# Kernel optimization log

Hardware: AMD Instinct MI355X
Metric: run time of the kernel (lower is better)

Reference implementation:

```python
import jax, jax.numpy as jnp
import numpy as np

BATCH, E = 4096, 8
DIMS = [512, 1024, 1024, 512]


def setup_inputs() -> dict:
    key = jax.random.key(0)
    ks = jax.random.split(key, 8)
    inp = {
        'weight_blend': jax.random.uniform(ks[0], (BATCH, E), dtype=jnp.float32),
        'x': jax.random.normal(ks[1], (BATCH, DIMS[0]), dtype=jnp.float32),
    }
    for i in range(3):
        inp[f'W{i}'] = jax.random.normal(ks[2 + i], (E, DIMS[i + 1], DIMS[i]), dtype=jnp.float32)
        inp[f'B{i}'] = jnp.zeros((E, DIMS[i + 1]), dtype=jnp.float32)
    return inp


def _blended_layer(weight_blend, x, W, B):
    # Fused form of: weight = sum_e blend[b,e]*W[e]; y = bmm(weight, x) + sum_e blend[b,e]*B[e]
    # Computed as sum_e blend_e * (W_e @ x) without materializing (batch,out,in).
    y = jnp.einsum('eoi,bi->beo', W, x)          # per-expert GEMM, (B,E,out)
    y = jnp.einsum('be,beo->bo', weight_blend, y)  # blend combine
    return y + weight_blend @ B                   # blended bias (B,out)


def reference(weight_blend, x, W0, B0, W1, B1, W2, B2):
    # Dropout with keep_prob=0.0 is identity in eval mode; activations: elu, elu, linear.
    h = jax.nn.elu(_blended_layer(weight_blend, x, W0, B0))
    h = jax.nn.elu(_blended_layer(weight_blend, h, W1, B1))
    out = _blended_layer(weight_blend, h, W2, B2)
    return out
```

## Files before the change

### kernel.cpp

```cpp
#include <hip/hip_runtime.h>
#include <cstdint>
#include <cstddef>

typedef __bf16 bf16x8 __attribute__((ext_vector_type(8)));
typedef float f32x4 __attribute__((ext_vector_type(4)));
typedef unsigned short u16;
typedef unsigned short u16x8 __attribute__((ext_vector_type(8)));

#define BATCH 4096
#define NE 8

__device__ __forceinline__ u16 f2bf(float f) {
  union { float f; uint32_t u; } v; v.f = f;
  uint32_t u = v.u;
  u += 0x7fffu + ((u >> 16) & 1u);
  return (u16)(u >> 16);
}

__device__ __forceinline__ float bf2f(u16 u) {
  union { uint32_t u; float f; } v; v.u = ((uint32_t)u) << 16;
  return v.f;
}

__device__ __forceinline__ void cast8(const float* src, u16* dst) {
  const float4* p = (const float4*)src;
  float4 a = p[0], b = p[1];
  u16x8 o;
  o[0] = f2bf(a.x); o[1] = f2bf(a.y); o[2] = f2bf(a.z); o[3] = f2bf(a.w);
  o[4] = f2bf(b.x); o[5] = f2bf(b.y); o[6] = f2bf(b.z); o[7] = f2bf(b.w);
  *(u16x8*)dst = o;
}

__device__ __forceinline__ void conv_w_chunk(const float* __restrict__ W,
                                             u16* __restrict__ Bt,
                                             int N, int K0, int chunk) {
  int per_row = K0 >> 3;
  int rid = chunk / per_row;
  int i0 = (chunk - rid * per_row) << 3;
  int e = rid / N;
  int o = rid - e * N;
  cast8(W + (size_t)rid * K0 + i0,
        Bt + (size_t)o * ((size_t)NE * K0) + (size_t)e * K0 + i0);
}

__global__ void prep_kernel(const float* __restrict__ x,
                            const float* __restrict__ W0,
                            const float* __restrict__ W1,
                            const float* __restrict__ W2,
                            u16* __restrict__ h0, u16* __restrict__ Bt0,
                            u16* __restrict__ Bt1, u16* __restrict__ Bt2) {
  int t = blockIdx.x * blockDim.x + threadIdx.x;
  const int C0 = BATCH * 512 / 8;
  const int C1 = C0 + NE * 1024 * 512 / 8;
  const int C2 = C1 + NE * 1024 * 1024 / 8;
  if (t < C0) {
    cast8(x + (size_t)t * 8, h0 + (size_t)t * 8);
  } else if (t < C1) {
    conv_w_chunk(W0, Bt0, 1024, 512, t - C0);
  } else if (t < C2) {
    conv_w_chunk(W1, Bt1, 1024, 1024, t - C1);
  } else {
    conv_w_chunk(W2, Bt2, 512, 1024, t - C2);
  }
}

template<int SLICES, bool ELU_ACT, bool OUT_BF16>
__global__ void combineS_kernel(const u16* __restrict__ P,
                                const float* __restrict__ blend,
                                const float* __restrict__ Bias,
                                void* __restrict__ outp, int N) {
  int t = blockIdx.x * blockDim.x + threadIdx.x;
  int per_row = N >> 3;
  int b = t / per_row;
  int i0 = (t - b * per_row) << 3;
  const size_t slice = (size_t)BATCH * N;
  float v[8] = {0, 0, 0, 0, 0, 0, 0, 0};
  #pragma unroll
  for (int s = 0; s < SLICES; ++s) {
    u16x8 pv = *(const u16x8*)(P + (size_t)s * slice + (size_t)b * N + i0);
    #pragma unroll
    for (int j = 0; j < 8; ++j) v[j] += bf2f(pv[j]);
  }
  const float4* blp = (const float4*)(blend + b * NE);
  float4 u0 = blp[0], u1 = blp[1];
  float bl[8] = {u0.x, u0.y, u0.z, u0.w, u1.x, u1.y, u1.z, u1.w};
  #pragma unroll
  for (int e = 0; e < NE; ++e) {
    const float4* bp = (const float4*)(Bias + (size_t)e * N + i0);
    float4 ba = bp[0], bb = bp[1];
    float bv[8] = {ba.x, ba.y, ba.z, ba.w, bb.x, bb.y, bb.z, bb.w};
    #pragma unroll
    for (int j = 0; j < 8; ++j) v[j] += bl[e] * bv[j];
  }
  if (ELU_ACT) {
    #pragma unroll
    for (int j = 0; j < 8; ++j) v[j] = v[j] > 0.f ? v[j] : expm1f(v[j]);
  }
  if (OUT_BF16) {
    u16x8 o;
    #pragma unroll
    for (int j = 0; j < 8; ++j) o[j] = f2bf(v[j]);
    *(u16x8*)((u16*)outp + (size_t)b * N + i0) = o;
  } else {
    float4* op = (float4*)((float*)outp + (size_t)b * N + i0);
    op[0] = (float4){v[0], v[1], v[2], v[3]};
    op[1] = (float4){v[4], v[5], v[6], v[7]};
  }
}

#define GL2LDS(g, l) __builtin_amdgcn_global_load_lds( \
    (__attribute__((address_space(1))) void*)(g),      \
    (__attribute__((address_space(3))) void*)(l), 16, 0, 0)

template<int K0, int EPB>
__global__ __launch_bounds__(256, 2)
void gemm_fold_kernel(const u16* __restrict__ h, const u16* __restrict__ Bt,
                      const float* __restrict__ blend,
                      u16* __restrict__ P, int N) {
  __shared__ __align__(16) u16 Hs[128 * 64];
  __shared__ __align__(16) u16 Bs[128 * 64];
  __shared__ float bls[128 * 9];

  const int tid  = threadIdx.x;
  const int w    = tid >> 6, lane = tid & 63;
  const int wm   = w >> 1,   wn   = w & 1;
  const int lrow = lane & 15, quad = lane >> 4;

  const int row0 = blockIdx.x * 128;
  const int col0 = blockIdx.y * 128;
  const int e0   = blockIdx.z * EPB;
  const int EK   = K0 * NE;

  {
    const float4 bv = ((const float4*)(blend + (size_t)row0 * NE))[tid];
    int row = tid >> 1, c0 = (tid & 1) * 4;
    bls[row * 9 + c0 + 0] = bv.x;
    bls[row * 9 + c0 + 1] = bv.y;
    bls[row * 9 + c0 + 2] = bv.z;
    bls[row * 9 + c0 + 3] = bv.w;
  }

  const int trow = tid >> 3;
  const int tcol = (tid & 7) ^ (trow & 7);
  const u16* gH = h + (size_t)(row0 + trow) * K0 + (tcol << 3);
  const u16* gB = Bt + (size_t)(col0 + trow) * EK + (size_t)e0 * K0 + (tcol << 3);
  u16* lH = &Hs[tid * 8];
  u16* lB = &Bs[tid * 8];

  const int xr = lrow & 7;
  const u16* fH[2][4];
  const u16* fB[2][4];
  #pragma unroll
  for (int kc = 0; kc < 2; ++kc)
    #pragma unroll
    for (int i = 0; i < 4; ++i) {
      fH[kc][i] = &Hs[(wm * 64 + i * 16 + lrow) * 64 + (((kc * 4 + quad) ^ xr) << 3)];
      fB[kc][i] = &Bs[(wn * 64 + i * 16 + lrow) * 64 + (((kc * 4 + quad) ^ xr) << 3)];
    }

  f32x4 acc[4][4];
  #pragma unroll
  for (int i = 0; i < 4; ++i)
    #pragma unroll
    for (int j = 0; j < 4; ++j) acc[i][j] = (f32x4){0.f, 0.f, 0.f, 0.f};

  #pragma unroll 1
  for (int ee = 0; ee < EPB; ++ee) {
    f32x4 acc2[4][4];
    #pragma unroll
    for (int i = 0; i < 4; ++i)
      #pragma unroll
      for (int j = 0; j < 4; ++j) acc2[i][j] = (f32x4){0.f, 0.f, 0.f, 0.f};

    const u16* pH = gH;
    const u16* pB = gB + (size_t)ee * K0;

    for (int it = 0; it < K0 / 64; ++it) {
      #pragma unroll
      for (int i = 0; i < 4; ++i) {
        GL2LDS(pH + (size_t)(32 * i) * K0, lH + 2048 * i);
        GL2LDS(pB + (size_t)(32 * i) * EK, lB + 2048 * i);
      }
      pH += 64; pB += 64;
      __syncthreads();

      #pragma unroll
      for (int kc = 0; kc < 2; ++kc) {
        bf16x8 hf[4], bfr[4];
        #pragma unroll
        for (int i = 0; i < 4; ++i) hf[i] = *(const bf16x8*)fH[kc][i];
        #pragma unroll
        for (int j = 0; j < 4; ++j) bfr[j] = *(const bf16x8*)fB[kc][j];
        #pragma unroll
        for (int i = 0; i < 4; ++i)
          #pragma unroll
          for (int j = 0; j < 4; ++j)
            acc2[i][j] = __builtin_amdgcn_mfma_f32_16x16x32_bf16(hf[i], bfr[j], acc2[i][j], 0, 0, 0);
      }
      __syncthreads();
    }

    #pragma unroll
    for (int mt = 0; mt < 4; ++mt) {
      float bl[4];
      #pragma unroll
      for (int r = 0; r < 4; ++r)
        bl[r] = bls[(wm * 64 + mt * 16 + quad * 4 + r) * 9 + (e0 + ee)];
      #pragma unroll
      for (int nt = 0; nt < 4; ++nt)
        #pragma unroll
        for (int r = 0; r < 4; ++r)
          acc[mt][nt][r] += bl[r] * acc2[mt][nt][r];
    }
  }

  u16* Ps = P + (size_t)blockIdx.z * ((size_t)BATCH * N);
  u16* ls = &Hs[w * 2048];
  #pragma unroll
  for (int half = 0; half < 2; ++half) {
    #pragma unroll
    for (int mh = 0; mh < 2; ++mh) {
      int mt = half * 2 + mh;
      #pragma unroll
      for (int r = 0; r < 4; ++r) {
        int rloc = mh * 16 + quad * 4 + r;
        #pragma unroll
        for (int nt = 0; nt < 4; ++nt) {
          int col = nt * 16 + lrow;
          int c8 = (col >> 3) ^ (rloc & 7);
          ls[rloc * 64 + (c8 << 3) + (col & 7)] = f2bf(acc[mt][nt][r]);
        }
      }
    }
    #pragma unroll
    for (int p = 0; p < 4; ++p) {
      int rloc = p * 8 + (lane >> 3);
      int c8 = (lane & 7) ^ (rloc & 7);
      u16x8 v = *(const u16x8*)&ls[rloc * 64 + (c8 << 3)];
      int row = row0 + wm * 64 + half * 32 + rloc;
      int colg = col0 + wn * 64 + ((lane & 7) << 3);
      *(u16x8*)&Ps[(size_t)row * N + colg] = v;
    }
  }
}

extern "C" void kernel_launch(void* const* d_in, const int* in_sizes, int n_in,
                              void* d_out, int out_size, void* d_ws, size_t ws_size,
                              hipStream_t stream) {
  const float* blend = (const float*)d_in[0];
  const float* x  = (const float*)d_in[1];
  const float* W0 = (const float*)d_in[2];
  const float* B0 = (const float*)d_in[3];
  const float* W1 = (const float*)d_in[4];
  const float* B1 = (const float*)d_in[5];
  const float* W2 = (const float*)d_in[6];
  const float* B2 = (const float*)d_in[7];
  float* out = (float*)d_out;

  char* ws = (char*)d_ws;
  u16* hA  = (u16*)ws;
  u16* h1  = (u16*)(ws + 8388608);
  u16* Bt0 = (u16*)(ws + 16777216);
  u16* Bt1 = (u16*)(ws + 25165824);
  u16* Bt2 = (u16*)(ws + 41943040);
  u16* P   = (u16*)(ws + 50331648);

  prep_kernel<<<9216, 256, 0, stream>>>(x, W0, W1, W2, hA, Bt0, Bt1, Bt2);

  gemm_fold_kernel<512, 4><<<dim3(32, 8, 2), 256, 0, stream>>>(hA, Bt0, blend, P, 1024);
  combineS_kernel<2, true, true><<<2048, 256, 0, stream>>>(P, blend, B0, h1, 1024);

  gemm_fold_kernel<1024, 4><<<dim3(32, 8, 2), 256, 0, stream>>>(h1, Bt1, blend, P, 1024);
  combineS_kernel<2, true, true><<<2048, 256, 0, stream>>>(P, blend, B1, hA, 1024);

  gemm_fold_kernel<1024, 2><<<dim3(32, 4, 4), 256, 0, stream>>>(hA, Bt2, blend, P, 512);
  combineS_kernel<4, false, false><<<1024, 256, 0, stream>>>(P, blend, B2, out, 512);
}
```

Measured before the change: 285.3 us.

## Pipeline blended GEMM with triple-buffered LDS and blend-scaled A tiles

Replaces the per-expert GEMM with an inner accumulator and epilogue blend by a single flattened K loop over experts. The blend weight is applied to the activation tile as it is written to LDS, so one accumulator suffices. The kernel uses 512 threads with a 256x128 tile, triple-buffered LDS, and register-staged A loads with explicit vmcnt waits, barriers and setprio, so global loads overlap MFMA work. In exchange, A values are rounded to bf16 after scaling, LDS use per block goes up, and occupancy may drop.

```diff
diff --git a/kernel.cpp b/kernel.cpp
--- a/kernel.cpp
+++ b/kernel.cpp
@@ -112,51 +112,79 @@
     (__attribute__((address_space(1))) void*)(g),      \
     (__attribute__((address_space(3))) void*)(l), 16, 0, 0)
 
+#define SBAR  asm volatile("s_barrier" ::: "memory")
+#define LGKM0 asm volatile("s_waitcnt lgkmcnt(0)" ::: "memory")
+#define VMW3  asm volatile("s_waitcnt vmcnt(3)" ::: "memory")
+#define VMW0  asm volatile("s_waitcnt vmcnt(0)" ::: "memory")
+
+__device__ __forceinline__ uint4 scale8(uint4 d, float s) {
+  uint32_t* pi = (uint32_t*)&d;
+  uint4 o;
+  uint32_t* po = (uint32_t*)&o;
+  #pragma unroll
+  for (int i = 0; i < 4; ++i) {
+    uint32_t wv = pi[i];
+    float lo = __uint_as_float(wv << 16) * s;
+    float hi = __uint_as_float(wv & 0xffff0000u) * s;
+    uint32_t pk;
+    asm("v_cvt_pk_bf16_f32 %0, %1, %2" : "=v"(pk) : "v"(lo), "v"(hi));
+    po[i] = pk;
+  }
+  return o;
+}
+
 template<int K0, int EPB>
-__global__ __launch_bounds__(256, 2)
-void gemm_fold_kernel(const u16* __restrict__ h, const u16* __restrict__ Bt,
+__global__ __launch_bounds__(512, 2)
+void gemm_pipe_kernel(const u16* __restrict__ h, const u16* __restrict__ Bt,
                       const float* __restrict__ blend,
                       u16* __restrict__ P, int N) {
-  __shared__ __align__(16) u16 Hs[128 * 64];
-  __shared__ __align__(16) u16 Bs[128 * 64];
-  __shared__ float bls[128 * 9];
+  constexpr int TPE  = K0 / 32;
+  constexpr int LTPE = (K0 == 512) ? 4 : 5;
+  constexpr int NT   = EPB * TPE;
+  const int EK = NE * K0;
+
+  __shared__ __align__(16) char SM[73728];
+  __shared__ float bls[256 * 9];
 
   const int tid  = threadIdx.x;
-  const int w    = tid >> 6, lane = tid & 63;
-  const int wm   = w >> 1,   wn   = w & 1;
+  const int lane = tid & 63, w = tid >> 6;
+  const int wm   = w >> 1, wn = w & 1;
   const int lrow = lane & 15, quad = lane >> 4;
 
-  const int row0 = blockIdx.x * 128;
+  const int row0 = blockIdx.x * 256;
   const int col0 = blockIdx.y * 128;
   const int e0   = blockIdx.z * EPB;
-  const int EK   = K0 * NE;
 
   {
     const float4 bv = ((const float4*)(blend + (size_t)row0 * NE))[tid];
-    int row = tid >> 1, c0 = (tid & 1) * 4;
-    bls[row * 9 + c0 + 0] = bv.x;
-    bls[row * 9 + c0 + 1] = bv.y;
-    bls[row * 9 + c0 + 2] = bv.z;
-    bls[row * 9 + c0 + 3] = bv.w;
-  }
-
-  const int trow = tid >> 3;
-  const int tcol = (tid & 7) ^ (trow & 7);
-  const u16* gH = h + (size_t)(row0 + trow) * K0 + (tcol << 3);
-  const u16* gB = Bt + (size_t)(col0 + trow) * EK + (size_t)e0 * K0 + (tcol << 3);
-  u16* lH = &Hs[tid * 8];
-  u16* lB = &Bs[tid * 8];
-
-  const int xr = lrow & 7;
-  const u16* fH[2][4];
-  const u16* fB[2][4];
-  #pragma unroll
-  for (int kc = 0; kc < 2; ++kc)
-    #pragma unroll
-    for (int i = 0; i < 4; ++i) {
-      fH[kc][i] = &Hs[(wm * 64 + i * 16 + lrow) * 64 + (((kc * 4 + quad) ^ xr) << 3)];
-      fB[kc][i] = &Bs[(wn * 64 + i * 16 + lrow) * 64 + (((kc * 4 + quad) ^ xr) << 3)];
-    }
+    int r = tid >> 1, c = (tid & 1) * 4;
+    bls[r * 9 + c + 0] = bv.x;
+    bls[r * 9 + c + 1] = bv.y;
+    bls[r * 9 + c + 2] = bv.z;
+    bls[r * 9 + c + 3] = bv.w;
+  }
+
+  const int sr  = tid >> 2, sc = tid & 3;
+  const int csw = sc ^ (sr & 3);
+  const uint32_t wA0 = (uint32_t)(sr * 64 + (csw << 4));
+  const uint32_t wA1 = (uint32_t)((128 + sr) * 64 + (csw << 4));
+  const int blo0 = sr * 9, blo1 = (128 + sr) * 9;
+
+  const u16* gA0 = h + (size_t)(row0 + sr) * K0 + sc * 8;
+  const u16* gA1 = gA0 + (size_t)128 * K0;
+  const u16* gB  = Bt + (size_t)(col0 + sr) * EK + csw * 8;
+
+#define KCOL(T) (((T) & (TPE - 1)) * 32)
+#define KOFF(T) ((e0 + ((T) >> LTPE)) * K0 + KCOL(T))
+
+  const int xq = quad ^ (lrow & 3);
+  uint32_t aoff[4], boff[4];
+  #pragma unroll
+  for (int i = 0; i < 4; ++i)
+    aoff[i] = (uint32_t)((wm * 64 + i * 16 + lrow) * 64 + (xq << 4));
+  #pragma unroll
+  for (int j = 0; j < 4; ++j)
+    boff[j] = (uint32_t)((wn * 64 + j * 16 + lrow) * 64 + (xq << 4));
 
   f32x4 acc[4][4];
   #pragma unroll
@@ -164,58 +192,81 @@
     #pragma unroll
     for (int j = 0; j < 4; ++j) acc[i][j] = (f32x4){0.f, 0.f, 0.f, 0.f};
 
+  __syncthreads();
+
+  uint32_t c0 = 0, c1 = 16384, c2 = 32768;
+  uint4 sE0, sE1, sO0, sO1;
+
+  GL2LDS(gB + KOFF(0), SM + 49152 + (c0 >> 1) + (size_t)tid * 16);
+  sE0 = *(const uint4*)(gA0 + KCOL(0));
+  sE1 = *(const uint4*)(gA1 + KCOL(0));
+  GL2LDS(gB + KOFF(1), SM + 49152 + (c1 >> 1) + (size_t)tid * 16);
+  sO0 = *(const uint4*)(gA0 + KCOL(1));
+  sO1 = *(const uint4*)(gA1 + KCOL(1));
+  {
+    const float bl0 = bls[blo0 + e0], bl1 = bls[blo1 + e0];
+    *(uint4*)(SM + c0 + wA0) = scale8(sE0, bl0);
+    *(uint4*)(SM + c0 + wA1) = scale8(sE1, bl1);
+  }
+  VMW0; LGKM0; SBAR;
+
+#define TILE(T, CUR, NXT, NN, LD0, LD1, WR0, WR1)                               \
+  {                                                                             \
+    bf16x8 bfr[4], afr[2];                                                      \
+    _Pragma("unroll")                                                           \
+    for (int j = 0; j < 4; ++j)                                                 \
+      bfr[j] = *(const bf16x8*)(SM + 49152 + ((CUR) >> 1) + boff[j]);           \
+    _Pragma("unroll")                                                           \
+    for (int i = 0; i < 2; ++i)                                                 \
+      afr[i] = *(const bf16x8*)(SM + (CUR) + aoff[i]);                          \
+    if ((T) + 2 < NT) {                                                         \
+      GL2LDS(gB + KOFF((T) + 2), SM + 49152 + ((NN) >> 1) + (size_t)tid * 16);  \
+      LD0 = *(const uint4*)(gA0 + KCOL((T) + 2));                               \
+      LD1 = *(const uint4*)(gA1 + KCOL((T) + 2));                               \
+    }                                                                           \
+    __builtin_amdgcn_s_setprio(1);                                              \
+    _Pragma("unroll")                                                           \
+    for (int i = 0; i < 2; ++i)                                                 \
+      _Pragma("unroll")                                                         \
+      for (int j = 0; j < 4; ++j)                                               \
+        acc[i][j] = __builtin_amdgcn_mfma_f32_16x16x32_bf16(afr[i], bfr[j],     \
+                                                            acc[i][j], 0, 0, 0);\
+    __builtin_amdgcn_s_setprio(0);                                              \
+    if ((T) + 1 < NT) {                                                         \
+      const int e_ = e0 + (((T) + 1) >> LTPE);                                  \
+      const float bl0_ = bls[blo0 + e_], bl1_ = bls[blo1 + e_];                 \
+      *(uint4*)(SM + (NXT) + wA0) = scale8(WR0, bl0_);                          \
+      *(uint4*)(SM + (NXT) + wA1) = scale8(WR1, bl1_);                          \
+    }                                                                           \
+    SBAR;                                                                       \
+    _Pragma("unroll")                                                           \
+    for (int i = 0; i < 2; ++i)                                                 \
+      afr[i] = *(const bf16x8*)(SM + (CUR) + aoff[2 + i]);                      \
+    __builtin_amdgcn_s_setprio(1);                                              \
+    _Pragma("unroll")                                                           \
+    for (int i = 0; i < 2; ++i)                                                 \
+      _Pragma("unroll")                                                         \
+      for (int j = 0; j < 4; ++j)                                               \
+        acc[2 + i][j] = __builtin_amdgcn_mfma_f32_16x16x32_bf16(                \
+            afr[i], bfr[j], acc[2 + i][j], 0, 0, 0);                            \
+    __builtin_amdgcn_s_setprio(0);                                              \
+    if ((T) + 2 < NT) { VMW3; } else { VMW0; }                                  \
+    LGKM0;                                                                      \
+    SBAR;                                                                       \
+  }
+
   #pragma unroll 1
-  for (int ee = 0; ee < EPB; ++ee) {
-    f32x4 acc2[4][4];
-    #pragma unroll
-    for (int i = 0; i < 4; ++i)
-      #pragma unroll
-      for (int j = 0; j < 4; ++j) acc2[i][j] = (f32x4){0.f, 0.f, 0.f, 0.f};
-
-    const u16* pH = gH;
-    const u16* pB = gB + (size_t)ee * K0;
-
-    for (int it = 0; it < K0 / 64; ++it) {
-      #pragma unroll
-      for (int i = 0; i < 4; ++i) {
-        GL2LDS(pH + (size_t)(32 * i) * K0, lH + 2048 * i);
-        GL2LDS(pB + (size_t)(32 * i) * EK, lB + 2048 * i);
-      }
-      pH += 64; pB += 64;
-      __syncthreads();
-
-      #pragma unroll
-      for (int kc = 0; kc < 2; ++kc) {
-        bf16x8 hf[4], bfr[4];
-        #pragma unroll
-        for (int i = 0; i < 4; ++i) hf[i] = *(const bf16x8*)fH[kc][i];
-        #pragma unroll
-        for (int j = 0; j < 4; ++j) bfr[j] = *(const bf16x8*)fB[kc][j];
-        #pragma unroll
-        for (int i = 0; i < 4; ++i)
-          #pragma unroll
-          for (int j = 0; j < 4; ++j)
-            acc2[i][j] = __builtin_amdgcn_mfma_f32_16x16x32_bf16(hf[i], bfr[j], acc2[i][j], 0, 0, 0);
-      }
-      __syncthreads();
-    }
-
-    #pragma unroll
-    for (int mt = 0; mt < 4; ++mt) {
-      float bl[4];
-      #pragma unroll
-      for (int r = 0; r < 4; ++r)
-        bl[r] = bls[(wm * 64 + mt * 16 + quad * 4 + r) * 9 + (e0 + ee)];
-      #pragma unroll
-      for (int nt = 0; nt < 4; ++nt)
-        #pragma unroll
-        for (int r = 0; r < 4; ++r)
-          acc[mt][nt][r] += bl[r] * acc2[mt][nt][r];
-    }
-  }
+  for (int t = 0; t < NT; t += 2) {
+    TILE(t,     c0, c1, c2, sE0, sE1, sO0, sO1);
+    TILE(t + 1, c1, c2, c0, sO0, sO1, sE0, sE1);
+    const uint32_t tmp = c2; c2 = c1; c1 = c0; c0 = tmp;
+  }
+#undef TILE
+#undef KOFF
+#undef KCOL
 
   u16* Ps = P + (size_t)blockIdx.z * ((size_t)BATCH * N);
-  u16* ls = &Hs[w * 2048];
+  u16* ls = (u16*)SM + w * 2048;
   #pragma unroll
   for (int half = 0; half < 2; ++half) {
     #pragma unroll
@@ -267,12 +318,12 @@
 
   prep_kernel<<<9216, 256, 0, stream>>>(x, W0, W1, W2, hA, Bt0, Bt1, Bt2);
 
-  gemm_fold_kernel<512, 4><<<dim3(32, 8, 2), 256, 0, stream>>>(hA, Bt0, blend, P, 1024);
+  gemm_pipe_kernel<512, 4><<<dim3(16, 8, 2), 512, 0, stream>>>(hA, Bt0, blend, P, 1024);
   combineS_kernel<2, true, true><<<2048, 256, 0, stream>>>(P, blend, B0, h1, 1024);
 
-  gemm_fold_kernel<1024, 4><<<dim3(32, 8, 2), 256, 0, stream>>>(h1, Bt1, blend, P, 1024);
+  gemm_pipe_kernel<1024, 4><<<dim3(16, 8, 2), 512, 0, stream>>>(h1, Bt1, blend, P, 1024);
   combineS_kernel<2, true, true><<<2048, 256, 0, stream>>>(P, blend, B1, hA, 1024);
 
-  gemm_fold_kernel<1024, 2><<<dim3(32, 4, 4), 256, 0, stream>>>(hA, Bt2, blend, P, 512);
+  gemm_pipe_kernel<1024, 2><<<dim3(16, 4, 4), 512, 0, stream>>>(hA, Bt2, blend, P, 512);
   combineS_kernel<4, false, false><<<1024, 256, 0, stream>>>(P, blend, B2, out, 512);
 }
```

Measured after the change: 376.7 us. 1.32x slower.

## Fold blend weights into expanded activations and use pipelined 256x256 split-K GEMM

Applied to the files above, without the earlier changes.

Pre-scales activations by each expert's blend weight (writing an expanded B x 8K bf16 activation), so each layer becomes a single plain GEMM over K=8*K0 against the expert-concatenated weights, with no per-expert epilogue. Replaces the old 128x128 GEMM with a 512-thread 256x256 tile kernel that double-buffers LDS with direct global-to-LDS loads, interleaved staging, explicit vmcnt waits and setprio, split across K slices. This removes the per-expert blend epilogue and improves data reuse and load/compute overlap. In exchange it multiplies activation memory traffic by 8 and needs more split-K partial slices in the combine step.

```diff
diff --git a/kernel.cpp b/kernel.cpp
--- a/kernel.cpp
+++ b/kernel.cpp
@@ -43,18 +43,33 @@
         Bt + (size_t)o * ((size_t)NE * K0) + (size_t)e * K0 + i0);
 }
 
-__global__ void prep_kernel(const float* __restrict__ x,
+__global__ void prep_kernel(const float* __restrict__ blend,
+                            const float* __restrict__ x,
                             const float* __restrict__ W0,
                             const float* __restrict__ W1,
                             const float* __restrict__ W2,
-                            u16* __restrict__ h0, u16* __restrict__ Bt0,
+                            u16* __restrict__ hh0, u16* __restrict__ Bt0,
                             u16* __restrict__ Bt1, u16* __restrict__ Bt2) {
   int t = blockIdx.x * blockDim.x + threadIdx.x;
   const int C0 = BATCH * 512 / 8;
   const int C1 = C0 + NE * 1024 * 512 / 8;
   const int C2 = C1 + NE * 1024 * 1024 / 8;
   if (t < C0) {
-    cast8(x + (size_t)t * 8, h0 + (size_t)t * 8);
+    int b = t >> 6, i0 = (t & 63) << 3;
+    const float4* xp = (const float4*)(x + (size_t)b * 512 + i0);
+    float4 a = xp[0], c = xp[1];
+    float xv[8] = {a.x, a.y, a.z, a.w, c.x, c.y, c.z, c.w};
+    const float4* blp = (const float4*)(blend + (size_t)b * NE);
+    float4 u0 = blp[0], u1 = blp[1];
+    float bl[8] = {u0.x, u0.y, u0.z, u0.w, u1.x, u1.y, u1.z, u1.w};
+    u16* dst = hh0 + (size_t)b * 4096 + i0;
+    #pragma unroll
+    for (int e = 0; e < NE; ++e) {
+      u16x8 o;
+      #pragma unroll
+      for (int j = 0; j < 8; ++j) o[j] = f2bf(bl[e] * xv[j]);
+      *(u16x8*)(dst + (size_t)e * 512) = o;
+    }
   } else if (t < C1) {
     conv_w_chunk(W0, Bt0, 1024, 512, t - C0);
   } else if (t < C2) {
@@ -64,7 +79,7 @@
   }
 }
 
-template<int SLICES, bool ELU_ACT, bool OUT_BF16>
+template<int SLICES, bool ELU_ACT, int OM>
 __global__ void combineS_kernel(const u16* __restrict__ P,
                                 const float* __restrict__ blend,
                                 const float* __restrict__ Bias,
@@ -96,11 +111,16 @@
     #pragma unroll
     for (int j = 0; j < 8; ++j) v[j] = v[j] > 0.f ? v[j] : expm1f(v[j]);
   }
-  if (OUT_BF16) {
-    u16x8 o;
-    #pragma unroll
-    for (int j = 0; j < 8; ++j) o[j] = f2bf(v[j]);
-    *(u16x8*)((u16*)outp + (size_t)b * N + i0) = o;
+  if (OM == 1) {
+    u16* hh = (u16*)outp;
+    size_t base = (size_t)b * ((size_t)NE * N) + i0;
+    #pragma unroll
+    for (int e = 0; e < NE; ++e) {
+      u16x8 o;
+      #pragma unroll
+      for (int j = 0; j < 8; ++j) o[j] = f2bf(bl[e] * v[j]);
+      *(u16x8*)(hh + base + (size_t)e * N) = o;
+    }
   } else {
     float4* op = (float4*)((float*)outp + (size_t)b * N + i0);
     op[0] = (float4){v[0], v[1], v[2], v[3]};
@@ -112,115 +132,121 @@
     (__attribute__((address_space(1))) void*)(g),      \
     (__attribute__((address_space(3))) void*)(l), 16, 0, 0)
 
-template<int K0, int EPB>
-__global__ __launch_bounds__(256, 2)
-void gemm_fold_kernel(const u16* __restrict__ h, const u16* __restrict__ Bt,
-                      const float* __restrict__ blend,
-                      u16* __restrict__ P, int N) {
-  __shared__ __align__(16) u16 Hs[128 * 64];
-  __shared__ __align__(16) u16 Bs[128 * 64];
-  __shared__ float bls[128 * 9];
+#define SBAR  asm volatile("s_barrier" ::: "memory")
+#define VMW6  asm volatile("s_waitcnt vmcnt(6)" ::: "memory")
+
+template<int NT>
+__global__ __launch_bounds__(512, 2)
+void gemm8p_kernel(const u16* __restrict__ A, const u16* __restrict__ B,
+                   u16* __restrict__ P, int N, int KTOT, int KSL) {
+  __shared__ __align__(16) char SM[131072];
 
   const int tid  = threadIdx.x;
-  const int w    = tid >> 6, lane = tid & 63;
-  const int wm   = w >> 1,   wn   = w & 1;
+  const int lane = tid & 63, w = tid >> 6;
+  const int wm   = w >> 2, wn = w & 3;
   const int lrow = lane & 15, quad = lane >> 4;
 
-  const int row0 = blockIdx.x * 128;
-  const int col0 = blockIdx.y * 128;
-  const int e0   = blockIdx.z * EPB;
-  const int EK   = K0 * NE;
-
-  {
-    const float4 bv = ((const float4*)(blend + (size_t)row0 * NE))[tid];
-    int row = tid >> 1, c0 = (tid & 1) * 4;
-    bls[row * 9 + c0 + 0] = bv.x;
-    bls[row * 9 + c0 + 1] = bv.y;
-    bls[row * 9 + c0 + 2] = bv.z;
-    bls[row * 9 + c0 + 3] = bv.w;
-  }
-
-  const int trow = tid >> 3;
-  const int tcol = (tid & 7) ^ (trow & 7);
-  const u16* gH = h + (size_t)(row0 + trow) * K0 + (tcol << 3);
-  const u16* gB = Bt + (size_t)(col0 + trow) * EK + (size_t)e0 * K0 + (tcol << 3);
-  u16* lH = &Hs[tid * 8];
-  u16* lB = &Bs[tid * 8];
+  const int row0 = blockIdx.x * 256;
+  const int col0 = blockIdx.y * 256;
+  const size_t kb0 = (size_t)blockIdx.z * KSL;
+
+  const int sr = tid >> 3, sc = tid & 7;
+  const int tcol = sc ^ (sr & 7);
+  const u16* gA = A + ((size_t)(row0 + sr) * KTOT + kb0 + (tcol << 3));
+  const u16* gB = B + ((size_t)(col0 + sr) * KTOT + kb0 + (tcol << 3));
+
+#define STA(T, q, BUF) GL2LDS(gA + (size_t)(64 * (q)) * KTOT + (size_t)(T) * 64, \
+                              SM + (BUF) * 65536 + (q) * 8192 + (size_t)tid * 16)
+#define STB(T, q, BUF) GL2LDS(gB + (size_t)(64 * (q)) * KTOT + (size_t)(T) * 64, \
+                              SM + (BUF) * 65536 + 32768 + (q) * 8192 + (size_t)tid * 16)
 
   const int xr = lrow & 7;
-  const u16* fH[2][4];
-  const u16* fB[2][4];
+  const uint32_t arow = (uint32_t)((wm * 128 + lrow) * 128);
+  const uint32_t brow = (uint32_t)((wn * 64 + lrow) * 128);
+  uint32_t ch[2];
+  ch[0] = (uint32_t)((quad ^ xr) << 4);
+  ch[1] = (uint32_t)(((4 + quad) ^ xr) << 4);
+
+  f32x4 acc[8][4];
   #pragma unroll
-  for (int kc = 0; kc < 2; ++kc)
-    #pragma unroll
-    for (int i = 0; i < 4; ++i) {
-      fH[kc][i] = &Hs[(wm * 64 + i * 16 + lrow) * 64 + (((kc * 4 + quad) ^ xr) << 3)];
-      fB[kc][i] = &Bs[(wn * 64 + i * 16 + lrow) * 64 + (((kc * 4 + quad) ^ xr) << 3)];
-    }
-
-  f32x4 acc[4][4];
+  for (int i = 0; i < 8; ++i)
+    #pragma unroll
+    for (int j = 0; j < 4; ++j) acc[i][j] = (f32x4){0.f, 0.f, 0.f, 0.f};
+
+  STA(0, 0, 0); STA(0, 1, 0); STA(0, 2, 0); STA(0, 3, 0);
+  STB(0, 0, 0); STB(0, 1, 0); STB(0, 2, 0); STB(0, 3, 0);
+  STB(1, 0, 1); STB(1, 1, 1); STB(1, 2, 1); STB(1, 3, 1);
+  STA(1, 0, 1); STA(1, 2, 1);
+  VMW6;
+  SBAR;
+
+#define PHASE(q, CUR, RDB, STAGES)                                              \
+  {                                                                             \
+    if (RDB) {                                                                  \
+      _Pragma("unroll")                                                         \
+      for (int nt = 0; nt < 4; ++nt)                                            \
+        _Pragma("unroll")                                                       \
+        for (int kc = 0; kc < 2; ++kc)                                          \
+          bfr[nt][kc] = *(const bf16x8*)(SM + (CUR) + 32768 + brow +            \
+                                         nt * 2048 + ch[kc]);                   \
+    }                                                                           \
+    bf16x8 af[2][2];                                                            \
+    _Pragma("unroll")                                                           \
+    for (int m2 = 0; m2 < 2; ++m2)                                              \
+      _Pragma("unroll")                                                         \
+      for (int kc = 0; kc < 2; ++kc)                                            \
+        af[m2][kc] = *(const bf16x8*)(SM + (CUR) + arow +                       \
+                                      ((q) * 2 + m2) * 2048 + ch[kc]);          \
+    STAGES;                                                                     \
+    SBAR;                                                                       \
+    __builtin_amdgcn_s_setprio(1);                                              \
+    _Pragma("unroll")                                                           \
+    for (int kc = 0; kc < 2; ++kc)                                              \
+      _Pragma("unroll")                                                         \
+      for (int m2 = 0; m2 < 2; ++m2)                                            \
+        _Pragma("unroll")                                                       \
+        for (int nt = 0; nt < 4; ++nt)                                          \
+          acc[(q) * 2 + m2][nt] = __builtin_amdgcn_mfma_f32_16x16x32_bf16(      \
+              af[m2][kc], bfr[nt][kc], acc[(q) * 2 + m2][nt], 0, 0, 0);         \
+    __builtin_amdgcn_s_setprio(0);                                              \
+  }
+
+  constexpr int NIT = NT / 2;
+  #pragma unroll 1
+  for (int j = 0; j < NIT; ++j) {
+    const int u = 2 * j;
+    const bool sg = (u + 2 < NT);
+    bf16x8 bfr[4][2];
+    PHASE(0, 0, true,  { STA(u + 1, 1, 1); STA(u + 1, 3, 1); });
+    SBAR;
+    PHASE(1, 0, false, { if (sg) { STB(u + 2, 0, 0); STB(u + 2, 1, 0); } });
+    SBAR;
+    PHASE(2, 0, false, { if (sg) { STA(u + 2, 0, 0); STA(u + 2, 2, 0); } });
+    SBAR;
+    PHASE(3, 0, false, { if (sg) { STB(u + 2, 2, 0); STB(u + 2, 3, 0); } });
+    VMW6;
+    SBAR;
+    PHASE(0, 65536, true,  { if (sg) { STA(u + 2, 1, 0); STA(u + 2, 3, 0); } });
+    SBAR;
+    PHASE(1, 65536, false, { if (sg) { STB(u + 3, 0, 1); STB(u + 3, 1, 1); } });
+    SBAR;
+    PHASE(2, 65536, false, { if (sg) { STA(u + 3, 0, 1); STA(u + 3, 2, 1); } });
+    SBAR;
+    PHASE(3, 65536, false, { if (sg) { STB(u + 3, 2, 1); STB(u + 3, 3, 1); } });
+    VMW6;
+    SBAR;
+  }
+#undef PHASE
+#undef STA
+#undef STB
+
+  u16* Ps = P + (size_t)blockIdx.z * ((size_t)BATCH * N);
+  u16* ls = (u16*)SM + w * 2048;
   #pragma unroll
-  for (int i = 0; i < 4; ++i)
-    #pragma unroll
-    for (int j = 0; j < 4; ++j) acc[i][j] = (f32x4){0.f, 0.f, 0.f, 0.f};
-
-  #pragma unroll 1
-  for (int ee = 0; ee < EPB; ++ee) {
-    f32x4 acc2[4][4];
-    #pragma unroll
-    for (int i = 0; i < 4; ++i)
-      #pragma unroll
-      for (int j = 0; j < 4; ++j) acc2[i][j] = (f32x4){0.f, 0.f, 0.f, 0.f};
-
-    const u16* pH = gH;
-    const u16* pB = gB + (size_t)ee * K0;
-
-    for (int it = 0; it < K0 / 64; ++it) {
-      #pragma unroll
-      for (int i = 0; i < 4; ++i) {
-        GL2LDS(pH + (size_t)(32 * i) * K0, lH + 2048 * i);
-        GL2LDS(pB + (size_t)(32 * i) * EK, lB + 2048 * i);
-      }
-      pH += 64; pB += 64;
-      __syncthreads();
-
-      #pragma unroll
-      for (int kc = 0; kc < 2; ++kc) {
-        bf16x8 hf[4], bfr[4];
-        #pragma unroll
-        for (int i = 0; i < 4; ++i) hf[i] = *(const bf16x8*)fH[kc][i];
-        #pragma unroll
-        for (int j = 0; j < 4; ++j) bfr[j] = *(const bf16x8*)fB[kc][j];
-        #pragma unroll
-        for (int i = 0; i < 4; ++i)
-          #pragma unroll
-          for (int j = 0; j < 4; ++j)
-            acc2[i][j] = __builtin_amdgcn_mfma_f32_16x16x32_bf16(hf[i], bfr[j], acc2[i][j], 0, 0, 0);
-      }
-      __syncthreads();
-    }
-
-    #pragma unroll
-    for (int mt = 0; mt < 4; ++mt) {
-      float bl[4];
-      #pragma unroll
-      for (int r = 0; r < 4; ++r)
-        bl[r] = bls[(wm * 64 + mt * 16 + quad * 4 + r) * 9 + (e0 + ee)];
-      #pragma unroll
-      for (int nt = 0; nt < 4; ++nt)
-        #pragma unroll
-        for (int r = 0; r < 4; ++r)
-          acc[mt][nt][r] += bl[r] * acc2[mt][nt][r];
-    }
-  }
-
-  u16* Ps = P + (size_t)blockIdx.z * ((size_t)BATCH * N);
-  u16* ls = &Hs[w * 2048];
-  #pragma unroll
-  for (int half = 0; half < 2; ++half) {
+  for (int pass = 0; pass < 4; ++pass) {
     #pragma unroll
     for (int mh = 0; mh < 2; ++mh) {
-      int mt = half * 2 + mh;
+      int mt = pass * 2 + mh;
       #pragma unroll
       for (int r = 0; r < 4; ++r) {
         int rloc = mh * 16 + quad * 4 + r;
@@ -233,11 +259,11 @@
       }
     }
     #pragma unroll
-    for (int p = 0; p < 4; ++p) {
-      int rloc = p * 8 + (lane >> 3);
+    for (int p8 = 0; p8 < 4; ++p8) {
+      int rloc = p8 * 8 + (lane >> 3);
       int c8 = (lane & 7) ^ (rloc & 7);
       u16x8 v = *(const u16x8*)&ls[rloc * 64 + (c8 << 3)];
-      int row = row0 + wm * 64 + half * 32 + rloc;
+      int row = row0 + wm * 128 + pass * 32 + rloc;
       int colg = col0 + wn * 64 + ((lane & 7) << 3);
       *(u16x8*)&Ps[(size_t)row * N + colg] = v;
     }
@@ -258,21 +284,22 @@
   float* out = (float*)d_out;
 
   char* ws = (char*)d_ws;
-  u16* hA  = (u16*)ws;
-  u16* h1  = (u16*)(ws + 8388608);
-  u16* Bt0 = (u16*)(ws + 16777216);
-  u16* Bt1 = (u16*)(ws + 25165824);
-  u16* Bt2 = (u16*)(ws + 41943040);
-  u16* P   = (u16*)(ws + 50331648);
-
-  prep_kernel<<<9216, 256, 0, stream>>>(x, W0, W1, W2, hA, Bt0, Bt1, Bt2);
-
-  gemm_fold_kernel<512, 4><<<dim3(32, 8, 2), 256, 0, stream>>>(hA, Bt0, blend, P, 1024);
-  combineS_kernel<2, true, true><<<2048, 256, 0, stream>>>(P, blend, B0, h1, 1024);
-
-  gemm_fold_kernel<1024, 4><<<dim3(32, 8, 2), 256, 0, stream>>>(h1, Bt1, blend, P, 1024);
-  combineS_kernel<2, true, true><<<2048, 256, 0, stream>>>(P, blend, B1, hA, 1024);
-
-  gemm_fold_kernel<1024, 2><<<dim3(32, 4, 4), 256, 0, stream>>>(hA, Bt2, blend, P, 512);
-  combineS_kernel<4, false, false><<<1024, 256, 0, stream>>>(P, blend, B2, out, 512);
-}
+  u16* hh1 = (u16*)ws;
+  u16* hh0 = (u16*)(ws + 67108864);
+  u16* hh2 = (u16*)(ws + 67108864);
+  u16* Bt0 = (u16*)(ws + 134217728);
+  u16* Bt1 = (u16*)(ws + 142606336);
+  u16* Bt2 = (u16*)(ws + 159383552);
+  u16* P   = (u16*)(ws + 167772160);
+
+  prep_kernel<<<9216, 256, 0, stream>>>(blend, x, W0, W1, W2, hh0, Bt0, Bt1, Bt2);
+
+  gemm8p_kernel<16><<<dim3(16, 4, 4), 512, 0, stream>>>(hh0, Bt0, P, 1024, 4096, 1024);
+  combineS_kernel<4, true, 1><<<2048, 256, 0, stream>>>(P, blend, B0, hh1, 1024);
+
+  gemm8p_kernel<32><<<dim3(16, 4, 4), 512, 0, stream>>>(hh1, Bt1, P, 1024, 8192, 2048);
+  combineS_kernel<4, true, 1><<<2048, 256, 0, stream>>>(P, blend, B1, hh2, 1024);
+
+  gemm8p_kernel<16><<<dim3(16, 2, 8), 512, 0, stream>>>(hh2, Bt2, P, 512, 8192, 1024);
+  combineS_kernel<8, false, 0><<<1024, 256, 0, stream>>>(P, blend, B2, out, 512);
+}
```

Result: slower. 304.7 us (+6.8%).

## Fuse all seven launches into one persistent cooperative kernel with grid barriers

Applied to the files above, without the earlier changes.

Replaces the prep, three GEMM and three combine launches with a single persistent kernel of 512 blocks that runs each phase in turn and separates phases with a software grid barrier built on atomics. The goal is to remove per-launch overhead and the idle gaps between kernels. In exchange, every phase is now limited to 512 blocks: prep and combine loop over their chunks in grid-stride fashion, and each barrier costs a spin on a global atomic. If the cooperative launch fails, the code falls back to a normal launch, which could deadlock if not all blocks are resident at once.

```diff
diff --git a/kernel.cpp b/kernel.cpp
--- a/kernel.cpp
+++ b/kernel.cpp
@@ -9,6 +9,7 @@
 
 #define BATCH 4096
 #define NE 8
+#define NBLK 512
 
 __device__ __forceinline__ u16 f2bf(float f) {
   union { float f; uint32_t u; } v; v.f = f;
@@ -30,6 +31,28 @@
   o[4] = f2bf(b.x); o[5] = f2bf(b.y); o[6] = f2bf(b.z); o[7] = f2bf(b.w);
   *(u16x8*)dst = o;
 }
+
+__device__ unsigned g_cnt = 0;
+__device__ unsigned g_gen = 0;
+
+__device__ __forceinline__ void gbar() {
+  __syncthreads();
+  if (threadIdx.x == 0) {
+    __threadfence();
+    unsigned my = __hip_atomic_load(&g_gen, __ATOMIC_RELAXED, __HIP_MEMORY_SCOPE_AGENT);
+    unsigned old = __hip_atomic_fetch_add(&g_cnt, 1u, __ATOMIC_ACQ_REL, __HIP_MEMORY_SCOPE_AGENT);
+    if (old == NBLK - 1u) {
+      __hip_atomic_store(&g_cnt, 0u, __ATOMIC_RELAXED, __HIP_MEMORY_SCOPE_AGENT);
+      __hip_atomic_fetch_add(&g_gen, 1u, __ATOMIC_RELEASE, __HIP_MEMORY_SCOPE_AGENT);
+    } else {
+      while (__hip_atomic_load(&g_gen, __ATOMIC_ACQUIRE, __HIP_MEMORY_SCOPE_AGENT) == my)
+        __builtin_amdgcn_s_sleep(8);
+    }
+    __threadfence();
+  }
+  __syncthreads();
+}
+
 
 __device__ __forceinline__ void conv_w_chunk(const float* __restrict__ W,
                                              u16* __restrict__ Bt,
@@ -43,13 +66,13 @@
         Bt + (size_t)o * ((size_t)NE * K0) + (size_t)e * K0 + i0);
 }
 
-__global__ void prep_kernel(const float* __restrict__ x,
-                            const float* __restrict__ W0,
-                            const float* __restrict__ W1,
-                            const float* __restrict__ W2,
-                            u16* __restrict__ h0, u16* __restrict__ Bt0,
-                            u16* __restrict__ Bt1, u16* __restrict__ Bt2) {
-  int t = blockIdx.x * blockDim.x + threadIdx.x;
+__device__ __forceinline__ void prep_chunk(const float* __restrict__ x,
+                                           const float* __restrict__ W0,
+                                           const float* __restrict__ W1,
+                                           const float* __restrict__ W2,
+                                           u16* __restrict__ h0, u16* __restrict__ Bt0,
+                                           u16* __restrict__ Bt1, u16* __restrict__ Bt2,
+                                           int t) {
   const int C0 = BATCH * 512 / 8;
   const int C1 = C0 + NE * 1024 * 512 / 8;
   const int C2 = C1 + NE * 1024 * 1024 / 8;
@@ -65,11 +88,10 @@
 }
 
 template<int SLICES, bool ELU_ACT, bool OUT_BF16>
-__global__ void combineS_kernel(const u16* __restrict__ P,
-                                const float* __restrict__ blend,
-                                const float* __restrict__ Bias,
-                                void* __restrict__ outp, int N) {
-  int t = blockIdx.x * blockDim.x + threadIdx.x;
+__device__ __forceinline__ void combine_chunk(const u16* __restrict__ P,
+                                              const float* __restrict__ blend,
+                                              const float* __restrict__ Bias,
+                                              void* __restrict__ outp, int N, int t) {
   int per_row = N >> 3;
   int b = t / per_row;
   int i0 = (t - b * per_row) << 3;
@@ -113,22 +135,22 @@
     (__attribute__((address_space(3))) void*)(l), 16, 0, 0)
 
 template<int K0, int EPB>
-__global__ __launch_bounds__(256, 2)
-void gemm_fold_kernel(const u16* __restrict__ h, const u16* __restrict__ Bt,
-                      const float* __restrict__ blend,
-                      u16* __restrict__ P, int N) {
-  __shared__ __align__(16) u16 Hs[128 * 64];
-  __shared__ __align__(16) u16 Bs[128 * 64];
-  __shared__ float bls[128 * 9];
+__device__ __forceinline__ void gemm_fold_phase(char* SMEM,
+    const u16* __restrict__ h, const u16* __restrict__ Bt,
+    const float* __restrict__ blend, u16* __restrict__ P, int N,
+    int bx, int by, int bz) {
+  u16* Hs   = (u16*)SMEM;
+  u16* Bs   = (u16*)(SMEM + 16384);
+  float* bls = (float*)(SMEM + 32768);
 
   const int tid  = threadIdx.x;
   const int w    = tid >> 6, lane = tid & 63;
   const int wm   = w >> 1,   wn   = w & 1;
   const int lrow = lane & 15, quad = lane >> 4;
 
-  const int row0 = blockIdx.x * 128;
-  const int col0 = blockIdx.y * 128;
-  const int e0   = blockIdx.z * EPB;
+  const int row0 = bx * 128;
+  const int col0 = by * 128;
+  const int e0   = bz * EPB;
   const int EK   = K0 * NE;
 
   {
@@ -214,7 +236,7 @@
     }
   }
 
-  u16* Ps = P + (size_t)blockIdx.z * ((size_t)BATCH * N);
+  u16* Ps = P + (size_t)bz * ((size_t)BATCH * N);
   u16* ls = &Hs[w * 2048];
   #pragma unroll
   for (int half = 0; half < 2; ++half) {
@@ -242,6 +264,52 @@
       *(u16x8*)&Ps[(size_t)row * N + colg] = v;
     }
   }
+}
+
+__global__ __launch_bounds__(256, 2)
+void fused_kernel(const float* __restrict__ blend, const float* __restrict__ x,
+                  const float* __restrict__ W0, const float* __restrict__ B0,
+                  const float* __restrict__ W1, const float* __restrict__ B1,
+                  const float* __restrict__ W2, const float* __restrict__ B2,
+                  float* __restrict__ out, char* __restrict__ ws) {
+  __shared__ __align__(16) char SMEM[37376];
+
+  u16* hA  = (u16*)ws;
+  u16* h1  = (u16*)(ws + 8388608);
+  u16* Bt0 = (u16*)(ws + 16777216);
+  u16* Bt1 = (u16*)(ws + 25165824);
+  u16* Bt2 = (u16*)(ws + 41943040);
+  u16* P   = (u16*)(ws + 50331648);
+
+  const int bid = blockIdx.x;
+  const int tid = threadIdx.x;
+
+  for (int i = bid; i < 9216; i += NBLK)
+    prep_chunk(x, W0, W1, W2, hA, Bt0, Bt1, Bt2, i * 256 + tid);
+  gbar();
+
+  gemm_fold_phase<512, 4>(SMEM, hA, Bt0, blend, P, 1024,
+                          bid & 31, (bid >> 5) & 7, bid >> 8);
+  gbar();
+
+  for (int i = bid; i < 2048; i += NBLK)
+    combine_chunk<2, true, true>(P, blend, B0, h1, 1024, i * 256 + tid);
+  gbar();
+
+  gemm_fold_phase<1024, 4>(SMEM, h1, Bt1, blend, P, 1024,
+                           bid & 31, (bid >> 5) & 7, bid >> 8);
+  gbar();
+
+  for (int i = bid; i < 2048; i += NBLK)
+    combine_chunk<2, true, true>(P, blend, B1, hA, 1024, i * 256 + tid);
+  gbar();
+
+  gemm_fold_phase<1024, 2>(SMEM, hA, Bt2, blend, P, 512,
+                           bid & 31, (bid >> 5) & 3, bid >> 7);
+  gbar();
+
+  for (int i = bid; i < 1024; i += NBLK)
+    combine_chunk<4, false, false>(P, blend, B2, out, 512, i * 256 + tid);
 }
 
 extern "C" void kernel_launch(void* const* d_in, const int* in_sizes, int n_in,
@@ -256,23 +324,14 @@
   const float* W2 = (const float*)d_in[6];
   const float* B2 = (const float*)d_in[7];
   float* out = (float*)d_out;
-
-  char* ws = (char*)d_ws;
-  u16* hA  = (u16*)ws;
-  u16* h1  = (u16*)(ws + 8388608);
-  u16* Bt0 = (u16*)(ws + 16777216);
-  u16* Bt1 = (u16*)(ws + 25165824);
-  u16* Bt2 = (u16*)(ws + 41943040);
-  u16* P   = (u16*)(ws + 50331648);
-
-  prep_kernel<<<9216, 256, 0, stream>>>(x, W0, W1, W2, hA, Bt0, Bt1, Bt2);
-
-  gemm_fold_kernel<512, 4><<<dim3(32, 8, 2), 256, 0, stream>>>(hA, Bt0, blend, P, 1024);
-  combineS_kernel<2, true, true><<<2048, 256, 0, stream>>>(P, blend, B0, h1, 1024);
-
-  gemm_fold_kernel<1024, 4><<<dim3(32, 8, 2), 256, 0, stream>>>(h1, Bt1, blend, P, 1024);
-  combineS_kernel<2, true, true><<<2048, 256, 0, stream>>>(P, blend, B1, hA, 1024);
-
-  gemm_fold_kernel<1024, 2><<<dim3(32, 4, 4), 256, 0, stream>>>(hA, Bt2, blend, P, 512);
-  combineS_kernel<4, false, false><<<1024, 256, 0, stream>>>(P, blend, B2, out, 512);
-}
+  char* wsp  = (char*)d_ws;
+
+  void* args[] = {&blend, &x, &W0, &B0, &W1, &B1, &W2, &B2, &out, &wsp};
+  hipError_t err = hipLaunchCooperativeKernel((const void*)fused_kernel,
+                                              dim3(NBLK), dim3(256),
+                                              args, 0, stream);
+  if (err != hipSuccess) {
+    fused_kernel<<<NBLK, 256, 0, stream>>>(blend, x, W0, B0, W1, B1, W2, B2,
+                                           out, wsp);
+  }
+}
```

Result: slower. 880.6 us (+208.7%).
